# Kernel tuning notes

Measured on AMD Instinct MI355X. Metric: run time of the kernel, lower is better.

The kernel has to match this reference:

```python
import jax, jax.numpy as jnp
import numpy as np

# Domain bounds and training nu-range (from init_kwargs)
X_MIN, X_MAX = -1.0, 1.0
Y_MIN, Y_MAX = -1.0, 1.0
T_MIN, T_MAX = 0.0, 1.0
NU_MIN, NU_MAX = 0.01, 0.1

LAYERS = [4, 256, 256, 256, 256, 2]
N = 16384  # collocation points


def setup_inputs() -> dict:
    key = jax.random.key(0)
    ks = jax.random.split(key, 4 + 2 * (len(LAYERS) - 1))
    inp = {
        'x': jax.random.uniform(ks[0], (N, 1), minval=X_MIN, maxval=X_MAX, dtype=jnp.float32),
        'y': jax.random.uniform(ks[1], (N, 1), minval=Y_MIN, maxval=Y_MAX, dtype=jnp.float32),
        't': jax.random.uniform(ks[2], (N, 1), minval=T_MIN, maxval=T_MAX, dtype=jnp.float32),
        'nu': jax.random.uniform(ks[3], (N, 1), minval=NU_MIN, maxval=NU_MAX, dtype=jnp.float32),
    }
    # glorot_normal weights, zero biases (keras Dense defaults)
    for i in range(len(LAYERS) - 1):
        fan_in, fan_out = LAYERS[i], LAYERS[i + 1]
        std = (2.0 / (fan_in + fan_out)) ** 0.5
        inp[f'W{i}'] = std * jax.random.normal(ks[4 + 2 * i], (fan_in, fan_out), dtype=jnp.float32)
        inp[f'b{i}'] = jnp.zeros((fan_out,), dtype=jnp.float32)
    return inp


def _net(pt, nu, params):
    """MLP forward for a single point. pt: (3,) = (x, y, t); nu: scalar. Returns (2,) = (u, v)."""
    x, y, t = pt[0], pt[1], pt[2]
    h = jnp.stack([
        2.0 * (x - X_MIN) / (X_MAX - X_MIN) - 1.0,
        2.0 * (y - Y_MIN) / (Y_MAX - Y_MIN) - 1.0,
        2.0 * (t - T_MIN) / (T_MAX - T_MIN) - 1.0,
        2.0 * (nu - NU_MIN) / (NU_MAX - NU_MIN) - 1.0,
    ])
    for W, b in params[:-1]:
        z = h @ W + b
        h = z * jax.nn.sigmoid(z)  # swish
    W, b = params[-1]
    return h @ W + b


def _residual_point(pt, nu, params):
    """Burgers PDE residual (f_u, f_v) at one collocation point via nested forward-mode AD."""
    f = lambda p: _net(p, nu, params)
    uv = f(pt)                          # (2,)
    J = jax.jacfwd(f)(pt)               # (2,3): d(u,v)/d(x,y,t)
    H = jax.jacfwd(jax.jacfwd(f))(pt)   # (2,3,3)
    u, v = uv[0], uv[1]
    u_x, u_y, u_t = J[0, 0], J[0, 1], J[0, 2]
    v_x, v_y, v_t = J[1, 0], J[1, 1], J[1, 2]
    u_xx, u_yy = H[0, 0, 0], H[0, 1, 1]
    v_xx, v_yy = H[1, 0, 0], H[1, 1, 1]
    f_u = u_t + u * u_x + v * u_y - nu * (u_xx + u_yy)
    f_v = v_t + u * v_x + v * v_y - nu * (v_xx + v_yy)
    return jnp.stack([f_u, f_v])


def reference(x, y, t, nu, W0, b0, W1, b1, W2, b2, W3, b3, W4, b4):
    params = [(W0, b0), (W1, b1), (W2, b2), (W3, b3), (W4, b4)]
    pts = jnp.concatenate([x, y, t], axis=1)  # (N, 3)
    res = jax.vmap(lambda p, n: _residual_point(p, n, params))(pts, nu[:, 0])
    return res  # (N, 2) = [f_u, f_v]
```

## Files before the change

kernel.cpp:

```cpp
#include <hip/hip_runtime.h>

typedef _Float16 f16;
typedef _Float16 v8hf __attribute__((ext_vector_type(8)));
typedef _Float16 v4hf __attribute__((ext_vector_type(4)));
typedef _Float16 v2hf __attribute__((ext_vector_type(2)));
typedef float    v4f  __attribute__((ext_vector_type(4)));

#define NPTS 16384
#define PTS  8
#define NLAYER_ELEMS 65536

__device__ __forceinline__ int swz(int m, int j) {
    return m * 256 + ((((j >> 3) ^ (m & 7)) << 3) | (j & 7));
}

__device__ __forceinline__ uint32_t pk_lo(float x0, float x1) {
    return __builtin_amdgcn_perm(__float_as_uint(x1), __float_as_uint(x0), 0x05040100u);
}
__device__ __forceinline__ uint32_t pk_hi(float x0, float x1) {
    return __builtin_amdgcn_perm(__float_as_uint(x1), __float_as_uint(x0), 0x07060302u);
}
__device__ __forceinline__ float up0(uint32_t lo, uint32_t hi) {
    return __uint_as_float(__builtin_amdgcn_perm(hi, lo, 0x05040100u));
}
__device__ __forceinline__ float up1(uint32_t lo, uint32_t hi) {
    return __uint_as_float(__builtin_amdgcn_perm(hi, lo, 0x07060302u));
}

__global__ void pack_weights(const float* __restrict__ W1, const float* __restrict__ W2,
                             const float* __restrict__ W3, f16* __restrict__ bh,
                             f16* __restrict__ bl) {
    const int b = blockIdx.x;
    const int L = b >> 5, r = b & 31, ks = r >> 2, i = r & 3;
    const int n = threadIdx.x;
    const float* W = (L == 0) ? W1 : (L == 1) ? W2 : W3;
    f16 h[8], l[8];
    #pragma unroll
    for (int j = 0; j < 8; ++j) {
        float w = W[(ks * 32 + i * 8 + j) * 256 + n];
        f16 hh = (f16)w;
        h[j] = hh;
        l[j] = (f16)(w - (float)hh);
    }
    size_t off = (size_t)L * NLAYER_ELEMS + (size_t)(ks * 256 + n) * 32 + (size_t)i * 8;
    *(v8hf*)(bh + off) = *(v8hf*)(h);
    *(v8hf*)(bl + off) = *(v8hf*)(l);
}

__global__ __launch_bounds__(256, 3) void pinn_burgers_kernel(
    const float* __restrict__ gx, const float* __restrict__ gy,
    const float* __restrict__ gt, const float* __restrict__ gnu,
    const float* __restrict__ W0, const float* __restrict__ b0,
    const float* __restrict__ b1, const float* __restrict__ b2,
    const float* __restrict__ b3,
    const float* __restrict__ W4, const float* __restrict__ b4,
    const f16* __restrict__ bh, const f16* __restrict__ bl,
    float* __restrict__ out)
{
    __shared__ f16 Ah[48 * 256];
    __shared__ f16 Al[48 * 256];
    __shared__ float red[PTS][12];
    __shared__ float pin[4][PTS];

    const int tid  = threadIdx.x;
    const int lane = tid & 63;
    const int wv   = tid >> 6;
    const int ln   = lane & 15;
    const int quad = lane >> 4;
    const int lnx  = ln & 7;
    const int p0   = blockIdx.x * PTS;

    const int k0w = lane * 4;
    const v4f w4a = *(const v4f*)(W4 + k0w * 2);
    const v4f w4b = *(const v4f*)(W4 + k0w * 2 + 4);
    const float b40 = b4[0], b41 = b4[1];

    if (tid < 4 * PTS) {
        int c = tid >> 3, p = tid & 7;
        const float* src = (c == 0) ? gx : (c == 1) ? gy : (c == 2) ? gt : gnu;
        pin[c][p] = src[p0 + p];
    }
    __syncthreads();

    const int pa    = lane >> 3;
    const int jb    = lane & 7;
    const int jbase = wv * 64 + jb * 8;

    auto ldw = [&](int Lidx, int ks, v8hf (&WH)[4], v8hf (&WL)[4]) {
        const f16* __restrict__ bhL = bh + (size_t)Lidx * NLAYER_ELEMS;
        const f16* __restrict__ blL = bl + (size_t)Lidx * NLAYER_ELEMS;
        #pragma unroll
        for (int t = 0; t < 4; ++t) {
            int n = wv * 64 + t * 16 + ln;
            size_t o = (size_t)(ks * 256 + n) * 32 + quad * 8;
            WH[t] = *(const v8hf*)(bhL + o);
            WL[t] = *(const v8hf*)(blL + o);
        }
    };
    v8hf wAh[4], wAl[4], wBh[4], wBl[4];

    auto store_split = [&](const float (&A)[8], int c) {
        v8hf hh, ll;
        #pragma unroll
        for (int e = 0; e < 8; ++e) {
            f16 hv = (f16)A[e];
            hh[e] = hv;
            ll[e] = (f16)(A[e] - (float)hv);
        }
        int idx = swz(c * PTS + pa, jbase);
        *(v8hf*)&Ah[idx] = hh;
        *(v8hf*)&Al[idx] = ll;
    };
    auto store_raw = [&](const float (&A)[8], int c) {
        uint4 lo, hi;
        lo.x = pk_lo(A[0], A[1]); lo.y = pk_lo(A[2], A[3]);
        lo.z = pk_lo(A[4], A[5]); lo.w = pk_lo(A[6], A[7]);
        hi.x = pk_hi(A[0], A[1]); hi.y = pk_hi(A[2], A[3]);
        hi.z = pk_hi(A[4], A[5]); hi.w = pk_hi(A[6], A[7]);
        int idx = swz(c * PTS + pa, jbase);
        *(uint4*)&Ah[idx] = lo;
        *(uint4*)&Al[idx] = hi;
    };

    {
        v4f w0v[2], w1v[2], w2v[2], w3v[2], bbv[2];
        #pragma unroll
        for (int h = 0; h < 2; ++h) {
            w0v[h] = *(const v4f*)(W0 +   0 + jbase + 4 * h);
            w1v[h] = *(const v4f*)(W0 + 256 + jbase + 4 * h);
            w2v[h] = *(const v4f*)(W0 + 512 + jbase + 4 * h);
            w3v[h] = *(const v4f*)(W0 + 768 + jbase + 4 * h);
            bbv[h] = *(const v4f*)(b0 + jbase + 4 * h);
        }
        float hx = pin[0][pa];
        float hy = pin[1][pa];
        float ht = 2.f * pin[2][pa] - 1.f;
        float hn = 2.f * (pin[3][pa] - 0.01f) * (1.f / 0.09f) - 1.f;
        float A0[8], A1[8], A2[8], A3[8], A4[8], A5[8];
        #pragma unroll
        for (int e = 0; e < 8; ++e) {
            float w0 = w0v[e >> 2][e & 3];
            float w1 = w1v[e >> 2][e & 3];
            float w2 = w2v[e >> 2][e & 3];
            float w3 = w3v[e >> 2][e & 3];
            float z  = hx * w0 + hy * w1 + ht * w2 + hn * w3 + bbv[e >> 2][e & 3];
            float zx = w0, zy = w1, zt = 2.f * w2;
            float s  = 1.f / (1.f + __expf(-z));
            float g1 = s * (1.f + z * (1.f - s));
            float g2 = s * (1.f - s) * (2.f + z * (1.f - 2.f * s));
            A0[e] = z * s;
            A1[e] = g1 * zx; A2[e] = g1 * zy; A3[e] = g1 * zt;
            A4[e] = g2 * zx * zx; A5[e] = g2 * zy * zy;
        }
        store_split(A0, 0); store_split(A1, 1); store_split(A2, 2);
        store_split(A3, 3); store_split(A4, 4); store_split(A5, 5);
    }
    ldw(0, 0, wAh, wAl);
    __syncthreads();

    const float* bias_ptr[3] = { b1, b2, b3 };
    #pragma unroll
    for (int L = 0; L < 3; ++L) {
        const float* __restrict__ bv = bias_ptr[L];

        v4f acc[4][3];
        #pragma unroll
        for (int t = 0; t < 4; ++t)
            #pragma unroll
            for (int mt = 0; mt < 3; ++mt)
                acc[t][mt] = (v4f){0.f, 0.f, 0.f, 0.f};

        #pragma unroll
        for (int ks = 0; ks < 8; ++ks) {
            if (ks < 7) {
                if (ks & 1) ldw(L, ks + 1, wAh, wAl);
                else        ldw(L, ks + 1, wBh, wBl);
            }
            const int cb = (((4 * ks + quad) ^ lnx) << 3);
            v8hf a_h[3], a_l[3];
            #pragma unroll
            for (int mt = 0; mt < 3; ++mt) {
                const int rb = (mt * 16 + ln) * 256 + cb;
                a_h[mt] = *(const v8hf*)&Ah[rb];
                a_l[mt] = *(const v8hf*)&Al[rb];
            }
            #pragma unroll
            for (int t = 0; t < 4; ++t)
                #pragma unroll
                for (int mt = 0; mt < 3; ++mt) {
                    const v8hf ch = (ks & 1) ? wBh[t] : wAh[t];
                    const v8hf cl = (ks & 1) ? wBl[t] : wAl[t];
                    acc[t][mt] = __builtin_amdgcn_mfma_f32_16x16x32_f16(ch, a_h[mt], acc[t][mt], 0, 0, 0);
                    acc[t][mt] = __builtin_amdgcn_mfma_f32_16x16x32_f16(ch, a_l[mt], acc[t][mt], 0, 0, 0);
                    acc[t][mt] = __builtin_amdgcn_mfma_f32_16x16x32_f16(cl, a_h[mt], acc[t][mt], 0, 0, 0);
                }
        }

        uint2 pkA[4][3], pkB[4][3];
        #pragma unroll
        for (int t = 0; t < 4; ++t)
            #pragma unroll
            for (int mt = 0; mt < 3; ++mt) {
                v4f a = acc[t][mt];
                int nb = wv * 64 + t * 16 + quad * 4;
                if (mt == 0 && ln < PTS) {
                    const float4 bq = *(const float4*)(bv + nb);
                    a[0] += bq.x; a[1] += bq.y; a[2] += bq.z; a[3] += bq.w;
                }
                pkA[t][mt] = (uint2){ pk_lo(a[0], a[1]), pk_lo(a[2], a[3]) };
                pkB[t][mt] = (uint2){ pk_hi(a[0], a[1]), pk_hi(a[2], a[3]) };
            }

        __syncthreads();

        #pragma unroll
        for (int t = 0; t < 4; ++t)
            #pragma unroll
            for (int mt = 0; mt < 3; ++mt) {
                const int nb  = wv * 64 + t * 16 + quad * 4;
                const int idx = swz(mt * 16 + ln, nb);
                *(uint2*)&Ah[idx] = pkA[t][mt];
                *(uint2*)&Al[idx] = pkB[t][mt];
            }

        if (L < 2) ldw(L + 1, 0, wAh, wAl);

        {
            float z0[8], z1[8], z2[8], z3[8], z4[8], z5[8];
            auto load_z = [&](float (&Z)[8], int c) {
                int idx = swz(c * PTS + pa, jbase);
                uint4 lo = *(const uint4*)&Ah[idx];
                uint4 hi = *(const uint4*)&Al[idx];
                Z[0] = up0(lo.x, hi.x); Z[1] = up1(lo.x, hi.x);
                Z[2] = up0(lo.y, hi.y); Z[3] = up1(lo.y, hi.y);
                Z[4] = up0(lo.z, hi.z); Z[5] = up1(lo.z, hi.z);
                Z[6] = up0(lo.w, hi.w); Z[7] = up1(lo.w, hi.w);
            };
            load_z(z0, 0); load_z(z1, 1); load_z(z2, 2);
            load_z(z3, 3); load_z(z4, 4); load_z(z5, 5);

            float A0[8], g1[8], g2[8];
            #pragma unroll
            for (int e = 0; e < 8; ++e) {
                float zz = z0[e];
                float s  = 1.f / (1.f + __expf(-zz));
                A0[e] = zz * s;
                g1[e] = s * (1.f + zz * (1.f - s));
                g2[e] = s * (1.f - s) * (2.f + zz * (1.f - 2.f * s));
            }
            float A1[8], A2[8], A3[8], A4[8], A5[8];
            #pragma unroll
            for (int e = 0; e < 8; ++e) {
                A1[e] = g1[e] * z1[e];
                A2[e] = g1[e] * z2[e];
                A3[e] = g1[e] * z3[e];
                A4[e] = g2[e] * z1[e] * z1[e] + g1[e] * z4[e];
                A5[e] = g2[e] * z2[e] * z2[e] + g1[e] * z5[e];
            }
            if (L < 2) {
                store_split(A0, 0); store_split(A1, 1); store_split(A2, 2);
                store_split(A3, 3); store_split(A4, 4); store_split(A5, 5);
            } else {
                store_raw(A0, 0); store_raw(A1, 1); store_raw(A2, 2);
                store_raw(A3, 3); store_raw(A4, 4); store_raw(A5, 5);
            }
        }
        __syncthreads();
    }

    #pragma unroll
    for (int d = 0; d < 24; ++d) {
        int D  = wv * 24 + d;
        int p  = D / 12;
        int rm = D % 12;
        int c  = rm >> 1;
        int o  = rm & 1;
        int m  = c * PTS + p;
        int idx = swz(m, k0w);
        uint2 lo = *(const uint2*)&Ah[idx];
        uint2 hi = *(const uint2*)&Al[idx];
        float h0 = up0(lo.x, hi.x), h1 = up1(lo.x, hi.x);
        float h2 = up0(lo.y, hi.y), h3 = up1(lo.y, hi.y);
        float partial = (o == 0)
            ? (h0 * w4a[0] + h1 * w4a[2] + h2 * w4b[0] + h3 * w4b[2])
            : (h0 * w4a[1] + h1 * w4a[3] + h2 * w4b[1] + h3 * w4b[3]);
        #pragma unroll
        for (int off = 32; off > 0; off >>= 1)
            partial += __shfl_down(partial, off);
        if (lane == 0)
            red[p][rm] = partial + ((c == 0) ? ((o == 0) ? b40 : b41) : 0.f);
    }
    __syncthreads();

    if (tid < PTS) {
        int p = tid;
        float u   = red[p][0],  v   = red[p][1];
        float ux  = red[p][2],  vx  = red[p][3];
        float uy  = red[p][4],  vy  = red[p][5];
        float ut  = red[p][6],  vt  = red[p][7];
        float uxx = red[p][8],  vxx = red[p][9];
        float uyy = red[p][10], vyy = red[p][11];
        float nuv = pin[3][p];
        float fu = ut + u * ux + v * uy - nuv * (uxx + uyy);
        float fv = vt + u * vx + v * vy - nuv * (vxx + vyy);
        out[(p0 + p) * 2 + 0] = fu;
        out[(p0 + p) * 2 + 1] = fv;
    }
}

extern "C" void kernel_launch(void* const* d_in, const int* in_sizes, int n_in,
                              void* d_out, int out_size, void* d_ws, size_t ws_size,
                              hipStream_t stream) {
    const float* x  = (const float*)d_in[0];
    const float* y  = (const float*)d_in[1];
    const float* t  = (const float*)d_in[2];
    const float* nu = (const float*)d_in[3];
    const float* W0 = (const float*)d_in[4];
    const float* b0 = (const float*)d_in[5];
    const float* W1 = (const float*)d_in[6];
    const float* b1 = (const float*)d_in[7];
    const float* W2 = (const float*)d_in[8];
    const float* b2 = (const float*)d_in[9];
    const float* W3 = (const float*)d_in[10];
    const float* b3 = (const float*)d_in[11];
    const float* W4 = (const float*)d_in[12];
    const float* b4 = (const float*)d_in[13];
    float* o = (float*)d_out;

    f16* bh = (f16*)d_ws;
    f16* bl = bh + 3 * (size_t)NLAYER_ELEMS;

    hipLaunchKernelGGL(pack_weights, dim3(96), dim3(256), 0, stream, W1, W2, W3, bh, bl);
    hipLaunchKernelGGL(pinn_burgers_kernel, dim3(NPTS / PTS), dim3(256), 0, stream,
                       x, y, t, nu, W0, b0, b1, b2, b3, W4, b4, bh, bl, o);
}
```

Measured before the change: 220.3 us.

## Drop register double-buffered weight prefetch; load weights inline with setprio

Removes the explicit A/B register double-buffering of weight fragments, which prefetched the next k-slice and the next layer's first slice. Weights are now loaded inside each k-step just before the MFMAs, which are wrapped in s_setprio. The layer loop is no longer fully unrolled and the k loop is unrolled by 2. This cuts register pressure and code size, which may raise occupancy, but global load latency is now exposed unless other waves hide it.

```diff
diff --git a/kernel.cpp b/kernel.cpp
--- a/kernel.cpp
+++ b/kernel.cpp
@@ -86,19 +86,6 @@
     const int jb    = lane & 7;
     const int jbase = wv * 64 + jb * 8;
 
-    auto ldw = [&](int Lidx, int ks, v8hf (&WH)[4], v8hf (&WL)[4]) {
-        const f16* __restrict__ bhL = bh + (size_t)Lidx * NLAYER_ELEMS;
-        const f16* __restrict__ blL = bl + (size_t)Lidx * NLAYER_ELEMS;
-        #pragma unroll
-        for (int t = 0; t < 4; ++t) {
-            int n = wv * 64 + t * 16 + ln;
-            size_t o = (size_t)(ks * 256 + n) * 32 + quad * 8;
-            WH[t] = *(const v8hf*)(bhL + o);
-            WL[t] = *(const v8hf*)(blL + o);
-        }
-    };
-    v8hf wAh[4], wAl[4], wBh[4], wBl[4];
-
     auto store_split = [&](const float (&A)[8], int c) {
         v8hf hh, ll;
         #pragma unroll
@@ -155,12 +142,12 @@
         store_split(A0, 0); store_split(A1, 1); store_split(A2, 2);
         store_split(A3, 3); store_split(A4, 4); store_split(A5, 5);
     }
-    ldw(0, 0, wAh, wAl);
     __syncthreads();
 
     const float* bias_ptr[3] = { b1, b2, b3 };
-    #pragma unroll
     for (int L = 0; L < 3; ++L) {
+        const f16* __restrict__ bhL = bh + (size_t)L * NLAYER_ELEMS;
+        const f16* __restrict__ blL = bl + (size_t)L * NLAYER_ELEMS;
         const float* __restrict__ bv = bias_ptr[L];
 
         v4f acc[4][3];
@@ -170,12 +157,8 @@
             for (int mt = 0; mt < 3; ++mt)
                 acc[t][mt] = (v4f){0.f, 0.f, 0.f, 0.f};
 
-        #pragma unroll
+        #pragma unroll 2
         for (int ks = 0; ks < 8; ++ks) {
-            if (ks < 7) {
-                if (ks & 1) ldw(L, ks + 1, wAh, wAl);
-                else        ldw(L, ks + 1, wBh, wBl);
-            }
             const int cb = (((4 * ks + quad) ^ lnx) << 3);
             v8hf a_h[3], a_l[3];
             #pragma unroll
@@ -184,16 +167,24 @@
                 a_h[mt] = *(const v8hf*)&Ah[rb];
                 a_l[mt] = *(const v8hf*)&Al[rb];
             }
+            v8hf w_h[4], w_l[4];
+            #pragma unroll
+            for (int t = 0; t < 4; ++t) {
+                int n = wv * 64 + t * 16 + ln;
+                size_t o = (size_t)(ks * 256 + n) * 32 + quad * 8;
+                w_h[t] = *(const v8hf*)(bhL + o);
+                w_l[t] = *(const v8hf*)(blL + o);
+            }
+            __builtin_amdgcn_s_setprio(1);
             #pragma unroll
             for (int t = 0; t < 4; ++t)
                 #pragma unroll
                 for (int mt = 0; mt < 3; ++mt) {
-                    const v8hf ch = (ks & 1) ? wBh[t] : wAh[t];
-                    const v8hf cl = (ks & 1) ? wBl[t] : wAl[t];
-                    acc[t][mt] = __builtin_amdgcn_mfma_f32_16x16x32_f16(ch, a_h[mt], acc[t][mt], 0, 0, 0);
-                    acc[t][mt] = __builtin_amdgcn_mfma_f32_16x16x32_f16(ch, a_l[mt], acc[t][mt], 0, 0, 0);
-                    acc[t][mt] = __builtin_amdgcn_mfma_f32_16x16x32_f16(cl, a_h[mt], acc[t][mt], 0, 0, 0);
+                    acc[t][mt] = __builtin_amdgcn_mfma_f32_16x16x32_f16(w_h[t], a_h[mt], acc[t][mt], 0, 0, 0);
+                    acc[t][mt] = __builtin_amdgcn_mfma_f32_16x16x32_f16(w_h[t], a_l[mt], acc[t][mt], 0, 0, 0);
+                    acc[t][mt] = __builtin_amdgcn_mfma_f32_16x16x32_f16(w_l[t], a_h[mt], acc[t][mt], 0, 0, 0);
                 }
+            __builtin_amdgcn_s_setprio(0);
         }
 
         uint2 pkA[4][3], pkB[4][3];
@@ -222,8 +213,6 @@
                 *(uint2*)&Ah[idx] = pkA[t][mt];
                 *(uint2*)&Al[idx] = pkB[t][mt];
             }
-
-        if (L < 2) ldw(L + 1, 0, wAh, wAl);
 
         {
             float z0[8], z1[8], z2[8], z3[8], z4[8], z5[8];
```

Measured after the change: 224.8 us. 1.02x slower.
